# Kernel optimization log

Measured on AMD Instinct MI355X. Metric: run time of the kernel, lower is better.

The kernel has to match this reference:

```python
import jax, jax.numpy as jnp
import numpy as np


def setup_inputs() -> dict:
    key = jax.random.key(0)
    k1, k2, k3 = jax.random.split(key, 3)
    B, H, S, D = 4, 16, 1024, 64
    return {
        "query": jax.random.normal(k1, (B, H, S, D), dtype=jnp.float32),
        "key": jax.random.normal(k2, (B, H, D, S), dtype=jnp.float32),  # pre-transposed K
        "scale_factor": 8,  # sqrt(head_dim)
        "attention_mask": jnp.zeros((S, S), dtype=jnp.float32),
        "value": jax.random.normal(k3, (B, H, S, D), dtype=jnp.float32),
    }


def reference(query, key, scale_factor, attention_mask, value):
    # Batched equivalent of the per-(b,h) Python loop:
    # scores = Q @ K^T / scale + mask; probs = softmax(scores); out = probs @ V
    scores = jnp.matmul(query, key) / scale_factor  # [B,H,S,S]
    if attention_mask is not None:
        scores = scores + attention_mask  # broadcast [S,S] over [B,H,S,S]
    probs = jax.nn.softmax(scores, axis=-1)
    return jnp.matmul(probs, value)  # [B,H,S,D]
```

## Files before the change

### kernel.cpp

```cpp
#include <hip/hip_runtime.h>

#define BH  64
#define SEQ 1024
#define DIM 64
#define KT  64
#define NT  (SEQ / KT)

typedef __attribute__((ext_vector_type(8))) short  short8;
typedef __attribute__((ext_vector_type(4))) float  floatx4;
typedef __attribute__((ext_vector_type(4))) uint   uintx4;

__device__ __forceinline__ ushort f2bf(float x) {
    union { float f; uint u; } v; v.f = x;
    uint r = v.u + 0x7FFFu + ((v.u >> 16) & 1u);
    return (ushort)(r >> 16);
}
__device__ __forceinline__ uint pack2(float lo, float hi) {
    return (uint)f2bf(lo) | ((uint)f2bf(hi) << 16);
}
__device__ __forceinline__ void gld_lds16(const void* g, void* l) {
    __builtin_amdgcn_global_load_lds(
        (const __attribute__((address_space(1))) unsigned int*)g,
        (__attribute__((address_space(3))) unsigned int*)l, 16, 0, 0);
}


__global__ __launch_bounds__(256) void prep_kv_kernel(
    const float* __restrict__ Kin,
    const float* __restrict__ Vin,
    ushort* __restrict__ Kbf, ushort* __restrict__ Vbf)
{
    __shared__ float tile[64][65];
    const int t    = threadIdx.x;
    const int head = blockIdx.y;
    const int s0   = blockIdx.x * 64;
    const int p    = t & 7;

    if (blockIdx.z == 0) {
        const float* ip = Kin + (size_t)head * DIM * SEQ;
#pragma unroll
        for (int i = 0; i < 4; ++i) {
            const int d = (t >> 4) + i * 16;
            const int c = (t & 15) * 4;
            float4 v = *(const float4*)(ip + (size_t)d * SEQ + s0 + c);
            tile[d][c]     = v.x; tile[d][c + 1] = v.y;
            tile[d][c + 2] = v.z; tile[d][c + 3] = v.w;
        }
        __syncthreads();
        char* op = (char*)(Kbf + (size_t)head * SEQ * DIM);
#pragma unroll
        for (int i = 0; i < 2; ++i) {
            const int s  = (t >> 3) + i * 32;
            const int dg = (p ^ (s & 7)) * 8;
            uint4 wv;
            wv.x = pack2(tile[dg + 0][s], tile[dg + 1][s]);
            wv.y = pack2(tile[dg + 2][s], tile[dg + 3][s]);
            wv.z = pack2(tile[dg + 4][s], tile[dg + 5][s]);
            wv.w = pack2(tile[dg + 6][s], tile[dg + 7][s]);
            *(uint4*)(op + (size_t)(s0 + s) * 128 + p * 16) = wv;
        }
    } else {
        const float* ip = Vin + (size_t)head * SEQ * DIM;
#pragma unroll
        for (int i = 0; i < 4; ++i) {
            const int ss = (t >> 4) + i * 16;
            const int c  = (t & 15) * 4;
            float4 v = *(const float4*)(ip + (size_t)(s0 + ss) * DIM + c);
            tile[ss][c]     = v.x; tile[ss][c + 1] = v.y;
            tile[ss][c + 2] = v.z; tile[ss][c + 3] = v.w;
        }
        __syncthreads();
        char* op = (char*)(Vbf + (size_t)head * SEQ * DIM) + (size_t)(s0 >> 6) * 8192;
#pragma unroll
        for (int i = 0; i < 2; ++i) {
            const int d  = (t >> 3) + i * 32;
            const int sg = (p ^ (d & 7)) * 8;
            uint4 wv;
            wv.x = pack2(tile[sg + 0][d], tile[sg + 1][d]);
            wv.y = pack2(tile[sg + 2][d], tile[sg + 3][d]);
            wv.z = pack2(tile[sg + 4][d], tile[sg + 5][d]);
            wv.w = pack2(tile[sg + 6][d], tile[sg + 7][d]);
            *(uint4*)(op + (size_t)d * 128 + p * 16) = wv;
        }
    }
}

__global__ __launch_bounds__(512, 4) void mha_mfma2_kernel(
    const float*  __restrict__ Q,
    const ushort* __restrict__ Kbf,
    const int*    __restrict__ scale_p,
    const float*  __restrict__ mask,
    const ushort* __restrict__ Vbf,
    float*        __restrict__ O)
{
    __shared__ __align__(16) ushort Ks0[KT * 64], Ks1[KT * 64];
    __shared__ __align__(16) ushort Vt0[DIM * 64], Vt1[DIM * 64];
    __shared__ __align__(16) ushort Ps[8 * 16 * 64];

    const int t    = threadIdx.x;
    const int lane = t & 63, w = t >> 6;
    const int li   = lane & 15, quad = lane >> 4;
    const int lx   = li & 7;
    const int bh   = blockIdx.x >> 3;
    const int q0   = (blockIdx.x & 7) * 128;

    const float inv_scale = 1.0f / (float)scale_p[0];

    short8 qa0, qa1;
    {
        const float* Qr = Q + ((size_t)bh * SEQ + q0 + w * 16 + li) * DIM + quad * 8;
        float4 a = *(const float4*)(Qr);
        float4 b = *(const float4*)(Qr + 4);
        float4 c = *(const float4*)(Qr + 32);
        float4 d = *(const float4*)(Qr + 36);
        qa0 = __builtin_bit_cast(short8,
              uintx4{pack2(a.x, a.y), pack2(a.z, a.w), pack2(b.x, b.y), pack2(b.z, b.w)});
        qa1 = __builtin_bit_cast(short8,
              uintx4{pack2(c.x, c.y), pack2(c.z, c.w), pack2(d.x, d.y), pack2(d.z, d.w)});
    }

    floatx4 o[4] = {floatx4{0,0,0,0}, floatx4{0,0,0,0},
                    floatx4{0,0,0,0}, floatx4{0,0,0,0}};
    float l_r[4] = {0.f, 0.f, 0.f, 0.f};

    const char* KgH = (const char*)(Kbf + (size_t)bh * SEQ * DIM);
    const char* VgH = (const char*)(Vbf + (size_t)bh * SEQ * DIM);
    const int so = w * 1024 + lane * 16;
    char* ksd0 = (char*)Ks0 + w * 1024;
    char* ksd1 = (char*)Ks1 + w * 1024;
    char* vtd0 = (char*)Vt0 + w * 1024;
    char* vtd1 = (char*)Vt1 + w * 1024;
    char* psw  = (char*)Ps  + w * 2048;

    const float* mrow = mask + (size_t)(q0 + w * 16 + quad * 4) * SEQ + li;

    float mvc[16], mvn[16];
#pragma unroll
    for (int n = 0; n < 4; ++n)
#pragma unroll
        for (int r = 0; r < 4; ++r)
            mvc[n * 4 + r] = mrow[(size_t)r * SEQ + n * 16];
    gld_lds16(KgH + so, ksd0);
    gld_lds16(VgH + so, vtd0);
    __builtin_amdgcn_sched_barrier(0);

#pragma unroll 2
    for (int kt = 0; kt < NT; ++kt) {
        const int c = kt & 1;
        const char* ksb = c ? (const char*)Ks1 : (const char*)Ks0;
        const char* vtb = c ? (const char*)Vt1 : (const char*)Vt0;
        char* ksdN = c ? ksd0 : ksd1;
        char* vtdN = c ? vtd0 : vtd1;

        __builtin_amdgcn_s_barrier();

        const int kn = (kt + 1) & (NT - 1);
#pragma unroll
        for (int n = 0; n < 4; ++n)
#pragma unroll
            for (int r = 0; r < 4; ++r)
                mvn[n * 4 + r] = mrow[(size_t)r * SEQ + kn * KT + n * 16];
        gld_lds16(KgH + kn * 8192 + so, ksdN);
        gld_lds16(VgH + kn * 8192 + so, vtdN);
        __builtin_amdgcn_sched_barrier(0);
        asm volatile("s_waitcnt vmcnt(18)" ::: "memory");
        __builtin_amdgcn_sched_barrier(0);
        __builtin_amdgcn_s_barrier();

        floatx4 cfr[4] = {floatx4{0,0,0,0}, floatx4{0,0,0,0},
                          floatx4{0,0,0,0}, floatx4{0,0,0,0}};
        __builtin_amdgcn_s_setprio(1);
#pragma unroll
        for (int n = 0; n < 4; ++n) {
            const char* krow = ksb + (n * 16 + li) * 128;
            short8 b0 = *(const short8*)(krow + ((quad ^ lx) * 16));
            short8 b1 = *(const short8*)(krow + (((4 + quad) ^ lx) * 16));
            cfr[n] = __builtin_amdgcn_mfma_f32_16x16x32_bf16(qa0, b0, cfr[n], 0, 0, 0);
            cfr[n] = __builtin_amdgcn_mfma_f32_16x16x32_bf16(qa1, b1, cfr[n], 0, 0, 0);
        }
        __builtin_amdgcn_s_setprio(0);

#pragma unroll
        for (int n = 0; n < 4; ++n)
#pragma unroll
            for (int r = 0; r < 4; ++r) {
                float s = fminf(fmaf(cfr[n][r], inv_scale, mvc[n * 4 + r]), 80.f);
                float p = __expf(s);
                l_r[r] += p;
                const int row = quad * 4 + r, col = n * 16 + li;
                *(ushort*)(psw + row * 128 + (((col >> 3) ^ (row & 7)) * 16)
                           + (col & 7) * 2) = f2bf(p);
            }

        __builtin_amdgcn_s_setprio(1);
#pragma unroll
        for (int kk = 0; kk < 2; ++kk) {
            short8 a = *(const short8*)(psw + li * 128 + (((kk * 4 + quad) ^ lx) * 16));
#pragma unroll
            for (int n = 0; n < 4; ++n) {
                const char* vrow = vtb + (n * 16 + li) * 128;
                short8 b = *(const short8*)(vrow + (((kk * 4 + quad) ^ lx) * 16));
                o[n] = __builtin_amdgcn_mfma_f32_16x16x32_bf16(a, b, o[n], 0, 0, 0);
            }
        }
        __builtin_amdgcn_s_setprio(0);

#pragma unroll
        for (int j = 0; j < 16; ++j) mvc[j] = mvn[j];
    }

#pragma unroll
    for (int off = 1; off < 16; off <<= 1)
#pragma unroll
        for (int r = 0; r < 4; ++r)
            l_r[r] += __shfl_xor(l_r[r], off);

    float* Og = O + ((size_t)bh * SEQ + q0) * DIM;
#pragma unroll
    for (int r = 0; r < 4; ++r) {
        const float inv_l = 1.0f / l_r[r];
#pragma unroll
        for (int n = 0; n < 4; ++n)
            Og[(size_t)(w * 16 + quad * 4 + r) * DIM + n * 16 + li] = o[n][r] * inv_l;
    }
}

extern "C" void kernel_launch(void* const* d_in, const int* in_sizes, int n_in,
                              void* d_out, int out_size, void* d_ws, size_t ws_size,
                              hipStream_t stream) {
    const float* Q     = (const float*)d_in[0];
    const float* K     = (const float*)d_in[1];
    const int*   scale = (const int*)d_in[2];
    const float* mask  = (const float*)d_in[3];
    const float* V     = (const float*)d_in[4];
    float*       Out   = (float*)d_out;

    ushort* Kbf = (ushort*)d_ws;
    ushort* Vbf = Kbf + (size_t)BH * SEQ * DIM;

    prep_kv_kernel<<<dim3(SEQ / 64, BH, 2), 256, 0, stream>>>(K, V, Kbf, Vbf);
    mha_mfma2_kernel<<<dim3(BH * (SEQ / 128)), 512, 0, stream>>>(Q, Kbf, scale, mask, Vbf, Out);
}
```

Measured before the change: 133.3 us.

## Compute transposed scores so P stays in registers, skip LDS round trip

```diff
diff --git a/kernel.cpp b/kernel.cpp
--- a/kernel.cpp
+++ b/kernel.cpp
@@ -17,6 +17,11 @@
 }
 __device__ __forceinline__ uint pack2(float lo, float hi) {
     return (uint)f2bf(lo) | ((uint)f2bf(hi) << 16);
+}
+__device__ __forceinline__ uint pk2(float lo, float hi) {
+    union { float f; uint u; } a, b; a.f = lo; b.f = hi;
+    uint au = a.u + 0x8000u, bu = b.u + 0x8000u;
+    return __builtin_amdgcn_perm(bu, au, 0x07060302);
 }
 __device__ __forceinline__ void gld_lds16(const void* g, void* l) {
     __builtin_amdgcn_global_load_lds(
@@ -74,28 +79,45 @@
 #pragma unroll
         for (int i = 0; i < 2; ++i) {
             const int d  = (t >> 3) + i * 32;
-            const int sg = (p ^ (d & 7)) * 8;
+            const int g  = p ^ (d & 7);
+            const int kb = ((g >> 2) * 32) + ((g & 3) * 4);
             uint4 wv;
-            wv.x = pack2(tile[sg + 0][d], tile[sg + 1][d]);
-            wv.y = pack2(tile[sg + 2][d], tile[sg + 3][d]);
-            wv.z = pack2(tile[sg + 4][d], tile[sg + 5][d]);
-            wv.w = pack2(tile[sg + 6][d], tile[sg + 7][d]);
+            wv.x = pack2(tile[kb +  0][d], tile[kb +  1][d]);
+            wv.y = pack2(tile[kb +  2][d], tile[kb +  3][d]);
+            wv.z = pack2(tile[kb + 16][d], tile[kb + 17][d]);
+            wv.w = pack2(tile[kb + 18][d], tile[kb + 19][d]);
             *(uint4*)(op + (size_t)d * 128 + p * 16) = wv;
         }
     }
+}
+
+__global__ __launch_bounds__(256) void prep_maskT_kernel(
+    const float* __restrict__ m, float* __restrict__ mt)
+{
+    __shared__ float tile[32][33];
+    const int t  = threadIdx.x;
+    const int k0 = blockIdx.x * 32;
+    const int q0 = blockIdx.y * 32;
+    const int tx = t & 31, ty = t >> 5;
+#pragma unroll
+    for (int i = 0; i < 4; ++i)
+        tile[ty + 8 * i][tx] = m[(size_t)(q0 + ty + 8 * i) * SEQ + k0 + tx];
+    __syncthreads();
+#pragma unroll
+    for (int i = 0; i < 4; ++i)
+        mt[(size_t)(k0 + ty + 8 * i) * SEQ + q0 + tx] = tile[tx][ty + 8 * i];
 }
 
 __global__ __launch_bounds__(512, 4) void mha_mfma2_kernel(
     const float*  __restrict__ Q,
     const ushort* __restrict__ Kbf,
     const int*    __restrict__ scale_p,
-    const float*  __restrict__ mask,
+    const float*  __restrict__ maskT,
     const ushort* __restrict__ Vbf,
     float*        __restrict__ O)
 {
     __shared__ __align__(16) ushort Ks0[KT * 64], Ks1[KT * 64];
     __shared__ __align__(16) ushort Vt0[DIM * 64], Vt1[DIM * 64];
-    __shared__ __align__(16) ushort Ps[8 * 16 * 64];
 
     const int t    = threadIdx.x;
     const int lane = t & 63, w = t >> 6;
@@ -121,7 +143,7 @@
 
     floatx4 o[4] = {floatx4{0,0,0,0}, floatx4{0,0,0,0},
                     floatx4{0,0,0,0}, floatx4{0,0,0,0}};
-    float l_r[4] = {0.f, 0.f, 0.f, 0.f};
+    float l = 0.f;
 
     const char* KgH = (const char*)(Kbf + (size_t)bh * SEQ * DIM);
     const char* VgH = (const char*)(Vbf + (size_t)bh * SEQ * DIM);
@@ -130,16 +152,15 @@
     char* ksd1 = (char*)Ks1 + w * 1024;
     char* vtd0 = (char*)Vt0 + w * 1024;
     char* vtd1 = (char*)Vt1 + w * 1024;
-    char* psw  = (char*)Ps  + w * 2048;
-
-    const float* mrow = mask + (size_t)(q0 + w * 16 + quad * 4) * SEQ + li;
+
+    const float* mrowT = maskT + (size_t)(quad * 4) * SEQ + q0 + w * 16 + li;
 
     float mvc[16], mvn[16];
 #pragma unroll
     for (int n = 0; n < 4; ++n)
 #pragma unroll
         for (int r = 0; r < 4; ++r)
-            mvc[n * 4 + r] = mrow[(size_t)r * SEQ + n * 16];
+            mvc[n * 4 + r] = mrowT[(size_t)(n * 16 + r) * SEQ];
     gld_lds16(KgH + so, ksd0);
     gld_lds16(VgH + so, vtd0);
     __builtin_amdgcn_sched_barrier(0);
@@ -159,7 +180,7 @@
         for (int n = 0; n < 4; ++n)
 #pragma unroll
             for (int r = 0; r < 4; ++r)
-                mvn[n * 4 + r] = mrow[(size_t)r * SEQ + kn * KT + n * 16];
+                mvn[n * 4 + r] = mrowT[(size_t)(kn * KT + n * 16 + r) * SEQ];
         gld_lds16(KgH + kn * 8192 + so, ksdN);
         gld_lds16(VgH + kn * 8192 + so, vtdN);
         __builtin_amdgcn_sched_barrier(0);
@@ -173,55 +194,55 @@
 #pragma unroll
         for (int n = 0; n < 4; ++n) {
             const char* krow = ksb + (n * 16 + li) * 128;
-            short8 b0 = *(const short8*)(krow + ((quad ^ lx) * 16));
-            short8 b1 = *(const short8*)(krow + (((4 + quad) ^ lx) * 16));
-            cfr[n] = __builtin_amdgcn_mfma_f32_16x16x32_bf16(qa0, b0, cfr[n], 0, 0, 0);
-            cfr[n] = __builtin_amdgcn_mfma_f32_16x16x32_bf16(qa1, b1, cfr[n], 0, 0, 0);
+            short8 kf0 = *(const short8*)(krow + ((quad ^ lx) * 16));
+            short8 kf1 = *(const short8*)(krow + (((4 + quad) ^ lx) * 16));
+            cfr[n] = __builtin_amdgcn_mfma_f32_16x16x32_bf16(kf0, qa0, cfr[n], 0, 0, 0);
+            cfr[n] = __builtin_amdgcn_mfma_f32_16x16x32_bf16(kf1, qa1, cfr[n], 0, 0, 0);
         }
         __builtin_amdgcn_s_setprio(0);
 
+        uint pw[8];
+#pragma unroll
+        for (int n = 0; n < 4; ++n) {
+            float p0 = __expf(fminf(fmaf(cfr[n][0], inv_scale, mvc[n * 4 + 0]), 80.f));
+            float p1 = __expf(fminf(fmaf(cfr[n][1], inv_scale, mvc[n * 4 + 1]), 80.f));
+            float p2 = __expf(fminf(fmaf(cfr[n][2], inv_scale, mvc[n * 4 + 2]), 80.f));
+            float p3 = __expf(fminf(fmaf(cfr[n][3], inv_scale, mvc[n * 4 + 3]), 80.f));
+            l += ((p0 + p1) + (p2 + p3));
+            pw[n * 2]     = pk2(p0, p1);
+            pw[n * 2 + 1] = pk2(p2, p3);
+        }
+        const short8 pa0 = __builtin_bit_cast(short8, uintx4{pw[0], pw[1], pw[2], pw[3]});
+        const short8 pa1 = __builtin_bit_cast(short8, uintx4{pw[4], pw[5], pw[6], pw[7]});
+
+        __builtin_amdgcn_s_setprio(1);
+#pragma unroll
+        for (int n = 0; n < 4; ++n) {
+            const char* vrow = vtb + (n * 16 + li) * 128;
+            short8 b0 = *(const short8*)(vrow + ((quad ^ lx) * 16));
+            short8 b1 = *(const short8*)(vrow + (((4 + quad) ^ lx) * 16));
+            o[n] = __builtin_amdgcn_mfma_f32_16x16x32_bf16(pa0, b0, o[n], 0, 0, 0);
+            o[n] = __builtin_amdgcn_mfma_f32_16x16x32_bf16(pa1, b1, o[n], 0, 0, 0);
+        }
+        __builtin_amdgcn_s_setprio(0);
+
+#pragma unroll
+        for (int j = 0; j < 16; ++j) mvc[j] = mvn[j];
+    }
+
+    l += __shfl_xor(l, 16);
+    l += __shfl_xor(l, 32);
+    float linv[4];
+#pragma unroll
+    for (int r = 0; r < 4; ++r)
+        linv[r] = 1.0f / __shfl(l, quad * 4 + r);
+
+    float* Og = O + ((size_t)bh * SEQ + q0) * DIM;
+#pragma unroll
+    for (int r = 0; r < 4; ++r) {
 #pragma unroll
         for (int n = 0; n < 4; ++n)
-#pragma unroll
-            for (int r = 0; r < 4; ++r) {
-                float s = fminf(fmaf(cfr[n][r], inv_scale, mvc[n * 4 + r]), 80.f);
-                float p = __expf(s);
-                l_r[r] += p;
-                const int row = quad * 4 + r, col = n * 16 + li;
-                *(ushort*)(psw + row * 128 + (((col >> 3) ^ (row & 7)) * 16)
-                           + (col & 7) * 2) = f2bf(p);
-            }
-
-        __builtin_amdgcn_s_setprio(1);
-#pragma unroll
-        for (int kk = 0; kk < 2; ++kk) {
-            short8 a = *(const short8*)(psw + li * 128 + (((kk * 4 + quad) ^ lx) * 16));
-#pragma unroll
-            for (int n = 0; n < 4; ++n) {
-                const char* vrow = vtb + (n * 16 + li) * 128;
-                short8 b = *(const short8*)(vrow + (((kk * 4 + quad) ^ lx) * 16));
-                o[n] = __builtin_amdgcn_mfma_f32_16x16x32_bf16(a, b, o[n], 0, 0, 0);
-            }
-        }
-        __builtin_amdgcn_s_setprio(0);
-
-#pragma unroll
-        for (int j = 0; j < 16; ++j) mvc[j] = mvn[j];
-    }
-
-#pragma unroll
-    for (int off = 1; off < 16; off <<= 1)
-#pragma unroll
-        for (int r = 0; r < 4; ++r)
-            l_r[r] += __shfl_xor(l_r[r], off);
-
-    float* Og = O + ((size_t)bh * SEQ + q0) * DIM;
-#pragma unroll
-    for (int r = 0; r < 4; ++r) {
-        const float inv_l = 1.0f / l_r[r];
-#pragma unroll
-        for (int n = 0; n < 4; ++n)
-            Og[(size_t)(w * 16 + quad * 4 + r) * DIM + n * 16 + li] = o[n][r] * inv_l;
+            Og[(size_t)(w * 16 + quad * 4 + r) * DIM + n * 16 + li] = o[n][r] * linv[r];
     }
 }
 
@@ -235,9 +256,11 @@
     const float* V     = (const float*)d_in[4];
     float*       Out   = (float*)d_out;
 
-    ushort* Kbf = (ushort*)d_ws;
-    ushort* Vbf = Kbf + (size_t)BH * SEQ * DIM;
+    ushort* Kbf   = (ushort*)d_ws;
+    ushort* Vbf   = Kbf + (size_t)BH * SEQ * DIM;
+    float*  maskT = (float*)((char*)d_ws + 2 * (size_t)BH * SEQ * DIM * 2);
 
     prep_kv_kernel<<<dim3(SEQ / 64, BH, 2), 256, 0, stream>>>(K, V, Kbf, Vbf);
-    mha_mfma2_kernel<<<dim3(BH * (SEQ / 128)), 512, 0, stream>>>(Q, Kbf, scale, mask, Vbf, Out);
-}
+    prep_maskT_kernel<<<dim3(SEQ / 32, SEQ / 32), 256, 0, stream>>>(mask, maskT);
+    mha_mfma2_kernel<<<dim3(BH * (SEQ / 128)), 512, 0, stream>>>(Q, Kbf, scale, maskT, Vbf, Out);
+}
```

Result: no change. 134.9 us (+1.2%).
